# Performance work log

Measured on AMD Instinct MI355X. Metric: run time of the kernel, lower is better.

## Reference

```python
import jax, jax.numpy as jnp
import numpy as np

V = 50000
E = 640000
DIM = 128
NUM_EDGE_TYPES = 32


def setup_inputs() -> dict:
    key = jax.random.key(0)
    ks = jax.random.split(key, 8)
    return {
        "node_values": jax.random.normal(ks[0], (V, DIM), dtype=jnp.float32),
        "edge_src": jax.random.randint(ks[1], (E,), 0, V, dtype=jnp.int32),
        "edge_dest": jax.random.randint(ks[2], (E,), 0, V, dtype=jnp.int32),
        "edge_cls": jax.random.randint(ks[3], (E,), 0, NUM_EDGE_TYPES, dtype=jnp.int32),
        "W_src": jax.random.normal(ks[4], (DIM, DIM), dtype=jnp.float32) / np.sqrt(DIM),
        "b_src": jnp.zeros((DIM,), dtype=jnp.float32),
        "W_dest": jax.random.normal(ks[5], (DIM, DIM), dtype=jnp.float32) / np.sqrt(DIM),
        "b_dest": jnp.zeros((DIM,), dtype=jnp.float32),
        "edge_emb": jax.random.normal(ks[6], (NUM_EDGE_TYPES, DIM), dtype=jnp.float32),
    }


def reference(node_values, edge_src, edge_dest, edge_cls, W_src, b_src, W_dest, b_dest, edge_emb):
    # Dense projections over all nodes, then gather per edge (matches tf.gather(dense(...), idx))
    src_proj = node_values @ W_src + b_src    # [V, dim]
    dest_proj = node_values @ W_dest + b_dest  # [V, dim]
    # Per-edge fused message: gather src, gather dest, edge-class embedding lookup, add, relu
    msgs = jax.nn.relu(src_proj[edge_src] + dest_proj[edge_dest] + edge_emb[edge_cls])  # [E, dim]
    # Scatter-reduce messages onto destination nodes
    out = jax.ops.segment_sum(msgs, edge_dest, num_segments=V)  # [V, dim]
    return out
```

## Files before the change

### kernel.cpp

```cpp
#include <hip/hip_runtime.h>


#define V 50000
#define E 640000
#define DIM 128
#define NRES 4
#define DRANGE 12500
#define NBIN_R 100
#define BINW 125
#define NBINS 400
#define BINCAP 2048
#define NE_MAX 896
#define QCAP 384
#define NCHUNK 256
#define EC4 625
#define NPROJ 782
#define NFUSED 1806

typedef __bf16 bf16x8 __attribute__((ext_vector_type(8)));
typedef float  f32x4  __attribute__((ext_vector_type(4)));
typedef float  f32x2  __attribute__((ext_vector_type(2)));

__device__ __forceinline__ float bf2f(unsigned int u16) {
    union { unsigned int i; float f; } c; c.i = u16 << 16; return c.f;
}
__device__ __forceinline__ unsigned int f2bf(float f) {
    union { float f; unsigned int i; } c; c.f = f;
    unsigned int u = c.i;
    return (u + 0x7FFFu + ((u >> 16) & 1u)) >> 16;
}

__global__ __launch_bounds__(256) void mp_setup(
    const float* __restrict__ Ws, const float* __restrict__ Wd,
    const float* __restrict__ emb,
    unsigned short* __restrict__ Wpk, unsigned short* __restrict__ embB,
    int* __restrict__ binCnt)
{
    int tid = blockIdx.x * 256 + threadIdx.x;
    int mat  = tid >> 11;
    int rem  = tid & 2047;
    int ct   = rem >> 8;
    int kt   = (rem >> 6) & 3;
    int lane = rem & 63;
    const float* W = mat ? Wd : Ws;
    int n  = ct * 16 + (lane & 15);
    int k0 = kt * 32 + (lane >> 4) * 8;
    unsigned short* dst = Wpk + (size_t)tid * 8;
    #pragma unroll
    for (int j = 0; j < 8; ++j) dst[j] = (unsigned short)f2bf(W[(k0 + j) * DIM + n]);
    embB[tid] = (unsigned short)f2bf(emb[tid]);
    if (tid < NBINS) binCnt[tid] = 0;
}

__global__ __launch_bounds__(256) void mp_fused(
    const int* __restrict__ ed, const int* __restrict__ es, const int* __restrict__ ec,
    int* __restrict__ binCnt, int* __restrict__ binbuf,
    const float* __restrict__ x, const unsigned short* __restrict__ Wpk,
    const float* __restrict__ bs, const float* __restrict__ bd,
    unsigned char* __restrict__ ps8, unsigned short* __restrict__ pdB)
{
    __shared__ float stage[4][16 * 132];

    const int b = blockIdx.x;
    const int t = threadIdx.x;
    const int r7 = b % 7;
    const bool isBin = (b < 1792) && (r7 < 4);

    if (isBin) {
        int* hist  = (int*)&stage[0][0];
        int* lofs  = hist + NBIN_R;
        int* lcur  = lofs + NBIN_R + 1;
        int* gbase = lcur + NBIN_R;
        int* csr   = gbase + NBIN_R;
        unsigned short* sbin = (unsigned short*)(csr + NE_MAX);

        const int a = (b / 7) * 4 + r7;
        const int r = a & (NRES - 1);
        const int c = a >> 2;
        const int dlo = r * DRANGE;

        if (t < NBIN_R) hist[t] = 0;

        int4 DV[3], SV[3], CV[3];
        {
            const int4* ed4 = (const int4*)ed + (size_t)c * EC4;
            const int4* es4 = (const int4*)es + (size_t)c * EC4;
            const int4* ec4 = (const int4*)ec + (size_t)c * EC4;
            #pragma unroll
            for (int k = 0; k < 3; ++k) {
                int i = t + k * 256;
                if (i < EC4) { DV[k] = ed4[i]; SV[k] = es4[i]; CV[k] = ec4[i]; }
                else { DV[k] = make_int4(-1, -1, -1, -1);
                       SV[k] = make_int4(0, 0, 0, 0); CV[k] = make_int4(0, 0, 0, 0); }
            }
        }
        __syncthreads();

        #pragma unroll
        for (int k = 0; k < 3; ++k) {
            #define H1(D) { int rel = (D) - dlo; \
                if ((unsigned)rel < DRANGE) atomicAdd(&hist[(unsigned)rel / BINW], 1); }
            H1(DV[k].x); H1(DV[k].y); H1(DV[k].z); H1(DV[k].w);
            #undef H1
        }
        __syncthreads();

        if (t < NBIN_R) gbase[t] = atomicAdd(&binCnt[r * NBIN_R + t], hist[t]);
        if (t < 64) {
            int carry = 0;
            #pragma unroll
            for (int s = 0; s < 2; ++s) {
                int idx = s * 64 + t;
                int v = (idx < NBIN_R) ? hist[idx] : 0;
                #pragma unroll
                for (int dlt = 1; dlt < 64; dlt <<= 1) {
                    int u = __shfl_up(v, dlt, 64);
                    if (t >= dlt) v += u;
                }
                int tot = __shfl(v, 63, 64);
                v += carry;
                if (idx < NBIN_R) { lofs[idx + 1] = v; lcur[idx] = v - hist[idx]; }
                carry += tot;
            }
            if (t == 0) lofs[0] = 0;
        }
        __syncthreads();

        #pragma unroll
        for (int k = 0; k < 3; ++k) {
            #define SC1(D, S, C) { int rel = (D) - dlo; \
                if ((unsigned)rel < DRANGE) { \
                    int bn = (unsigned)rel / BINW; \
                    int rl = rel - bn * BINW; \
                    int pos = atomicAdd(&lcur[bn], 1); \
                    if (pos < NE_MAX) { \
                        csr[pos] = ((S) & 0xFFFF) | ((C) << 16) | (rl << 21); \
                        sbin[pos] = (unsigned short)bn; } } }
            SC1(DV[k].x, SV[k].x, CV[k].x); SC1(DV[k].y, SV[k].y, CV[k].y);
            SC1(DV[k].z, SV[k].z, CV[k].z); SC1(DV[k].w, SV[k].w, CV[k].w);
            #undef SC1
        }
        __syncthreads();

        int ne = lofs[NBIN_R]; if (ne > NE_MAX) ne = NE_MAX;

        for (int i = t; i < ne; i += 256) {
            int bb = sbin[i];
            int slot = gbase[bb] + (i - lofs[bb]);
            if (slot < BINCAP)
                binbuf[(size_t)(r * NBIN_R + bb) * BINCAP + slot] = csr[i];
        }
        return;
    }

    const int p = (b < 1792) ? ((b / 7) * 3 + (r7 - 4)) : (768 + (b - 1792));
    if (p >= NPROJ) return;
    const int wave = __builtin_amdgcn_readfirstlane(threadIdx.x) >> 6;
    const int lane = threadIdx.x & 63;
    const int m = lane & 15, q = lane >> 4;
    const int row0 = p * 64 + wave * 16;

    int arow = row0 + m; if (arow >= V) arow = V - 1;
    const float* xr = x + (size_t)arow * DIM + q * 8;

    bf16x8 A[4];
    #pragma unroll
    for (int kt = 0; kt < 4; ++kt) {
        float4 u = *(const float4*)(xr + kt * 32);
        float4 v = *(const float4*)(xr + kt * 32 + 4);
        bf16x8 a;
        a[0] = (__bf16)u.x; a[1] = (__bf16)u.y; a[2] = (__bf16)u.z; a[3] = (__bf16)u.w;
        a[4] = (__bf16)v.x; a[5] = (__bf16)v.y; a[6] = (__bf16)v.z; a[7] = (__bf16)v.w;
        A[kt] = a;
    }

    const bf16x8* Bp = (const bf16x8*)Wpk;

    f32x4 accS[8], accD[8];
    #pragma unroll
    for (int ct = 0; ct < 8; ++ct) {
        f32x4 aS = {0.f, 0.f, 0.f, 0.f}, aD = {0.f, 0.f, 0.f, 0.f};
        #pragma unroll
        for (int kt = 0; kt < 4; ++kt) {
            bf16x8 bS = Bp[((0 * 8 + ct) * 4 + kt) * 64 + lane];
            bf16x8 bD = Bp[((1 * 8 + ct) * 4 + kt) * 64 + lane];
            aS = __builtin_amdgcn_mfma_f32_16x16x32_bf16(A[kt], bS, aS, 0, 0, 0);
            aD = __builtin_amdgcn_mfma_f32_16x16x32_bf16(A[kt], bD, aD, 0, 0, 0);
        }
        accS[ct] = aS; accD[ct] = aD;
    }

    float* st = stage[wave];
    const int rr = lane & 15, cg = lane >> 4;
    const int orow = row0 + rr;
    const float* rowp = st + rr * 132 + cg * 32;

    #pragma unroll
    for (int ct = 0; ct < 8; ++ct) {
        const float bv = bs[ct * 16 + m];
        #pragma unroll
        for (int rg = 0; rg < 4; ++rg)
            st[(q * 4 + rg) * 132 + ct * 16 + m] = accS[ct][rg] + bv;
    }
    __syncthreads();
    {
        int w[8];
        #pragma unroll
        for (int j = 0; j < 8; ++j) {
            float4 f = *(const float4*)(rowp + 4 * j);
            int v = __builtin_amdgcn_cvt_pk_fp8_f32(f.x, f.y, 0, false);
            v = __builtin_amdgcn_cvt_pk_fp8_f32(f.z, f.w, v, true);
            w[j] = v;
        }
        if (orow < V) {
            int4* dst = (int4*)(ps8 + (size_t)orow * 128 + cg * 32);
            dst[0] = make_int4(w[0], w[1], w[2], w[3]);
            dst[1] = make_int4(w[4], w[5], w[6], w[7]);
        }
    }
    __syncthreads();

    #pragma unroll
    for (int ct = 0; ct < 8; ++ct) {
        const float bv = bd[ct * 16 + m];
        #pragma unroll
        for (int rg = 0; rg < 4; ++rg)
            st[(q * 4 + rg) * 132 + ct * 16 + m] = accD[ct][rg] + bv;
    }
    __syncthreads();
    {
        int w[16];
        #pragma unroll
        for (int j = 0; j < 8; ++j) {
            float4 f = *(const float4*)(rowp + 4 * j);
            w[2 * j]     = f2bf(f.x) | (f2bf(f.y) << 16);
            w[2 * j + 1] = f2bf(f.z) | (f2bf(f.w) << 16);
        }
        if (orow < V) {
            int4* dst = (int4*)(pdB + (size_t)orow * 128 + cg * 32);
            #pragma unroll
            for (int jj = 0; jj < 4; ++jj)
                dst[jj] = make_int4(w[4 * jj], w[4 * jj + 1], w[4 * jj + 2], w[4 * jj + 3]);
        }
    }
}

__global__ __launch_bounds__(256) void mp_binBC(
    const unsigned char* __restrict__ ps8, const unsigned short* __restrict__ pdB,
    const unsigned short* __restrict__ embB,
    const int* __restrict__ binCnt, const int* __restrict__ binbuf,
    float* __restrict__ out)
{
    __shared__ int csr[QCAP];
    __shared__ int cnt[16];
    __shared__ int off[17];
    __shared__ int cur[16];
    __shared__ unsigned short sEmb[32 * DIM];

    const int bin = blockIdx.x >> 3;
    const int qu = blockIdx.x & 7;
    const int rel0 = qu * 16;
    const int relW = (qu == 7) ? 13 : 16;
    const int d0 = bin * BINW + rel0;
    const int t = threadIdx.x;
    const int wave = t >> 6, lane = t & 63;

    int nb = binCnt[bin]; if (nb > BINCAP) nb = BINCAP;
    const int* buf = binbuf + (size_t)bin * BINCAP;

    if (t < 16) cnt[t] = 0;

    {
        const int4* s4 = (const int4*)embB;
        int4* d4 = (int4*)sEmb;
        d4[t] = s4[t];
        d4[t + 256] = s4[t + 256];
    }

    int EB[8];
    #pragma unroll
    for (int k = 0; k < 8; ++k) {
        int i = t + k * 256;
        EB[k] = (i < nb) ? buf[i] : -1;
    }

    float dp0v[4], dp1v[4];
    #pragma unroll
    for (int k = 0; k < 4; ++k) {
        int rl = wave + k * 4;
        int d = d0 + ((rl < relW) ? rl : 0);
        unsigned int pdu = *(const unsigned int*)(pdB + (size_t)d * DIM + 2 * lane);
        dp0v[k] = bf2f(pdu & 0xFFFF); dp1v[k] = bf2f(pdu >> 16);
    }
    __syncthreads();

    #pragma unroll
    for (int k = 0; k < 8; ++k) {
        int rl = (int)((unsigned)EB[k] >> 21) - rel0;
        if ((unsigned)rl < (unsigned)relW) atomicAdd(&cnt[rl], 1);
    }
    __syncthreads();

    if (t < 16) {
        int v = (t < relW) ? cnt[t] : 0;
        #pragma unroll
        for (int dlt = 1; dlt < 16; dlt <<= 1) {
            int u = __shfl_up(v, dlt, 64);
            if (t >= dlt) v += u;
        }
        off[t + 1] = v;
        cur[t] = v - cnt[t];
        if (t == 0) off[0] = 0;
    }
    __syncthreads();

    #pragma unroll
    for (int k = 0; k < 8; ++k) {
        int rl = (int)((unsigned)EB[k] >> 21) - rel0;
        if ((unsigned)rl < (unsigned)relW) {
            int pos = atomicAdd(&cur[rl], 1);
            if (pos < QCAP) csr[pos] = EB[k];
        }
    }
    __syncthreads();

    #define PROC(P) { \
        int s_ = *(const unsigned short*)(ps8 + ((size_t)((P) & 0xFFFF) << 7) + 2 * lane); \
        unsigned int e_ = *(const unsigned int*)(sEmb + ((((P) >> 16) & 0x1F) << 7) + 2 * lane); \
        f32x2 f_ = __builtin_amdgcn_cvt_pk_f32_fp8(s_, false); \
        a0 += fmaxf(f_.x + dp0 + bf2f(e_ & 0xFFFF), 0.f); \
        a1 += fmaxf(f_.y + dp1 + bf2f(e_ >> 16),    0.f); }

    #pragma unroll
    for (int k = 0; k < 4; ++k) {
        const int rl = wave + k * 4;
        if (rl >= relW) break;
        const int d = d0 + rl;
        int i0 = off[rl], i1 = off[rl + 1];
        if (i1 > QCAP) i1 = QCAP;
        if (i0 > i1) i0 = i1;
        const float dp0 = dp0v[k], dp1 = dp1v[k];
        float a0 = 0.f, a1 = 0.f;
        int i = i0;
        for (; i + 8 <= i1; i += 8) {
            int p0 = csr[i],     p1 = csr[i + 1], p2 = csr[i + 2], p3 = csr[i + 3];
            int p4 = csr[i + 4], p5 = csr[i + 5], p6 = csr[i + 6], p7 = csr[i + 7];
            PROC(p0); PROC(p1); PROC(p2); PROC(p3);
            PROC(p4); PROC(p5); PROC(p6); PROC(p7);
        }
        for (; i + 4 <= i1; i += 4) {
            int p0 = csr[i], p1 = csr[i + 1], p2 = csr[i + 2], p3 = csr[i + 3];
            PROC(p0); PROC(p1); PROC(p2); PROC(p3);
        }
        for (; i < i1; ++i) { int p0 = csr[i]; PROC(p0); }
        *(float2*)(out + (size_t)d * DIM + 2 * lane) = make_float2(a0, a1);
    }
    #undef PROC
}

extern "C" void kernel_launch(void* const* d_in, const int* in_sizes, int n_in,
                              void* d_out, int out_size, void* d_ws, size_t ws_size,
                              hipStream_t stream) {
    const float* x   = (const float*)d_in[0];
    const int*   es  = (const int*)d_in[1];
    const int*   ed  = (const int*)d_in[2];
    const int*   ec  = (const int*)d_in[3];
    const float* Ws  = (const float*)d_in[4];
    const float* bs  = (const float*)d_in[5];
    const float* Wd  = (const float*)d_in[6];
    const float* bd  = (const float*)d_in[7];
    const float* emb = (const float*)d_in[8];
    float* out = (float*)d_out;

    char* ws = (char*)d_ws;
    size_t off = 0;
    unsigned char*  ps8  = (unsigned char*)(ws + off);  off += (size_t)V * 128;
    unsigned short* pdB  = (unsigned short*)(ws + off); off += (size_t)V * DIM * 2;
    int* binbuf = (int*)(ws + off);                     off += (size_t)NBINS * BINCAP * 4;
    int* binCnt = (int*)(ws + off);                     off += (size_t)NBINS * 4;
    unsigned short* Wpk  = (unsigned short*)(ws + off); off += 2 * 128 * 128 * 2;
    unsigned short* embB = (unsigned short*)(ws + off); off += 32 * 128 * 2;

    mp_setup<<<16, 256, 0, stream>>>(Ws, Wd, emb, Wpk, embB, binCnt);
    mp_fused<<<NFUSED, 256, 0, stream>>>(ed, es, ec, binCnt, binbuf,
                                         x, Wpk, bs, bd, ps8, pdB);
    mp_binBC<<<NBINS * 8, 256, 0, stream>>>(ps8, pdB, embB, binCnt, binbuf, out);
}
```

Measured before the change: 155.0 us.

## Bin all destinations per edge chunk in one pass and XCD-map bin blocks

```diff
diff --git a/kernel.cpp b/kernel.cpp
--- a/kernel.cpp
+++ b/kernel.cpp
@@ -4,18 +4,17 @@
 #define V 50000
 #define E 640000
 #define DIM 128
-#define NRES 4
-#define DRANGE 12500
-#define NBIN_R 100
+#define NXCD 8
+#define NBIN_R 50
 #define BINW 125
 #define NBINS 400
 #define BINCAP 2048
-#define NE_MAX 896
 #define QCAP 384
 #define NCHUNK 256
+#define CSRN 2500
 #define EC4 625
 #define NPROJ 782
-#define NFUSED 1806
+#define NFUSED 1038
 
 typedef __bf16 bf16x8 __attribute__((ext_vector_type(8)));
 typedef float  f32x4  __attribute__((ext_vector_type(4)));
@@ -63,23 +62,20 @@
 
     const int b = blockIdx.x;
     const int t = threadIdx.x;
-    const int r7 = b % 7;
-    const bool isBin = (b < 1792) && (r7 < 4);
+    const bool isBin = ((b & 3) == 3) && (b < 1024);
 
     if (isBin) {
-        int* hist  = (int*)&stage[0][0];
-        int* lofs  = hist + NBIN_R;
-        int* lcur  = lofs + NBIN_R + 1;
-        int* gbase = lcur + NBIN_R;
-        int* csr   = gbase + NBIN_R;
-        unsigned short* sbin = (unsigned short*)(csr + NE_MAX);
-
-        const int a = (b / 7) * 4 + r7;
-        const int r = a & (NRES - 1);
-        const int c = a >> 2;
-        const int dlo = r * DRANGE;
-
-        if (t < NBIN_R) hist[t] = 0;
+        int* base  = (int*)&stage[0][0];
+        int* hist  = base;
+        int* lofs  = base + 400;
+        int* lcur  = base + 801;
+        int* gbase = base + 1201;
+        int* csr   = base + 1601;
+        unsigned short* sbin = (unsigned short*)(base + 4101);
+
+        const int c = b >> 2;
+
+        for (int i = t; i < NBINS; i += 256) hist[i] = 0;
 
         int4 DV[3], SV[3], CV[3];
         {
@@ -98,20 +94,20 @@
 
         #pragma unroll
         for (int k = 0; k < 3; ++k) {
-            #define H1(D) { int rel = (D) - dlo; \
-                if ((unsigned)rel < DRANGE) atomicAdd(&hist[(unsigned)rel / BINW], 1); }
+            #define H1(D) if ((D) >= 0) atomicAdd(&hist[(unsigned)(D) / BINW], 1);
             H1(DV[k].x); H1(DV[k].y); H1(DV[k].z); H1(DV[k].w);
             #undef H1
         }
         __syncthreads();
 
-        if (t < NBIN_R) gbase[t] = atomicAdd(&binCnt[r * NBIN_R + t], hist[t]);
+        for (int i = t; i < NBINS; i += 256)
+            gbase[i] = atomicAdd(&binCnt[i], hist[i]);
         if (t < 64) {
             int carry = 0;
             #pragma unroll
-            for (int s = 0; s < 2; ++s) {
+            for (int s = 0; s < 7; ++s) {
                 int idx = s * 64 + t;
-                int v = (idx < NBIN_R) ? hist[idx] : 0;
+                int v = (idx < NBINS) ? hist[idx] : 0;
                 #pragma unroll
                 for (int dlt = 1; dlt < 64; dlt <<= 1) {
                     int u = __shfl_up(v, dlt, 64);
@@ -119,7 +115,7 @@
                 }
                 int tot = __shfl(v, 63, 64);
                 v += carry;
-                if (idx < NBIN_R) { lofs[idx + 1] = v; lcur[idx] = v - hist[idx]; }
+                if (idx < NBINS) { lofs[idx + 1] = v; lcur[idx] = v - hist[idx]; }
                 carry += tot;
             }
             if (t == 0) lofs[0] = 0;
@@ -128,32 +124,28 @@
 
         #pragma unroll
         for (int k = 0; k < 3; ++k) {
-            #define SC1(D, S, C) { int rel = (D) - dlo; \
-                if ((unsigned)rel < DRANGE) { \
-                    int bn = (unsigned)rel / BINW; \
-                    int rl = rel - bn * BINW; \
-                    int pos = atomicAdd(&lcur[bn], 1); \
-                    if (pos < NE_MAX) { \
-                        csr[pos] = ((S) & 0xFFFF) | ((C) << 16) | (rl << 21); \
-                        sbin[pos] = (unsigned short)bn; } } }
+            #define SC1(D, S, C) if ((D) >= 0) { \
+                int bn = (unsigned)(D) / BINW; \
+                int rl = (D) - bn * BINW; \
+                int pos = atomicAdd(&lcur[bn], 1); \
+                csr[pos] = ((S) & 0xFFFF) | ((C) << 16) | (rl << 21); \
+                sbin[pos] = (unsigned short)bn; }
             SC1(DV[k].x, SV[k].x, CV[k].x); SC1(DV[k].y, SV[k].y, CV[k].y);
             SC1(DV[k].z, SV[k].z, CV[k].z); SC1(DV[k].w, SV[k].w, CV[k].w);
             #undef SC1
         }
         __syncthreads();
 
-        int ne = lofs[NBIN_R]; if (ne > NE_MAX) ne = NE_MAX;
-
-        for (int i = t; i < ne; i += 256) {
+        for (int i = t; i < CSRN; i += 256) {
             int bb = sbin[i];
             int slot = gbase[bb] + (i - lofs[bb]);
             if (slot < BINCAP)
-                binbuf[(size_t)(r * NBIN_R + bb) * BINCAP + slot] = csr[i];
+                binbuf[(size_t)bb * BINCAP + slot] = csr[i];
         }
         return;
     }
 
-    const int p = (b < 1792) ? ((b / 7) * 3 + (r7 - 4)) : (768 + (b - 1792));
+    const int p = (b < 1024) ? (b - ((b + 1) >> 2)) : (b - 256);
     if (p >= NPROJ) return;
     const int wave = __builtin_amdgcn_readfirstlane(threadIdx.x) >> 6;
     const int lane = threadIdx.x & 63;
@@ -255,10 +247,12 @@
     __shared__ int cnt[16];
     __shared__ int off[17];
     __shared__ int cur[16];
-    __shared__ unsigned short sEmb[32 * DIM];
-
-    const int bin = blockIdx.x >> 3;
-    const int qu = blockIdx.x & 7;
+
+    const int r = blockIdx.x & (NXCD - 1);
+    const int rest = blockIdx.x >> 3;
+    const int bi = rest % NBIN_R;
+    const int qu = rest / NBIN_R;
+    const int bin = r * NBIN_R + bi;
     const int rel0 = qu * 16;
     const int relW = (qu == 7) ? 13 : 16;
     const int d0 = bin * BINW + rel0;
@@ -270,13 +264,6 @@
 
     if (t < 16) cnt[t] = 0;
 
-    {
-        const int4* s4 = (const int4*)embB;
-        int4* d4 = (int4*)sEmb;
-        d4[t] = s4[t];
-        d4[t + 256] = s4[t + 256];
-    }
-
     int EB[8];
     #pragma unroll
     for (int k = 0; k < 8; ++k) {
@@ -326,7 +313,7 @@
 
     #define PROC(P) { \
         int s_ = *(const unsigned short*)(ps8 + ((size_t)((P) & 0xFFFF) << 7) + 2 * lane); \
-        unsigned int e_ = *(const unsigned int*)(sEmb + ((((P) >> 16) & 0x1F) << 7) + 2 * lane); \
+        unsigned int e_ = *(const unsigned int*)(embB + ((((P) >> 16) & 0x1F) << 7) + 2 * lane); \
         f32x2 f_ = __builtin_amdgcn_cvt_pk_f32_fp8(s_, false); \
         a0 += fmaxf(f_.x + dp0 + bf2f(e_ & 0xFFFF), 0.f); \
         a1 += fmaxf(f_.y + dp1 + bf2f(e_ >> 16),    0.f); }
@@ -384,5 +371,5 @@
     mp_setup<<<16, 256, 0, stream>>>(Ws, Wd, emb, Wpk, embB, binCnt);
     mp_fused<<<NFUSED, 256, 0, stream>>>(ed, es, ec, binCnt, binbuf,
                                          x, Wpk, bs, bd, ps8, pdB);
-    mp_binBC<<<NBINS * 8, 256, 0, stream>>>(ps8, pdB, embB, binCnt, binbuf, out);
-}
+    mp_binBC<<<NBIN_R * NXCD * 8, 256, 0, stream>>>(ps8, pdB, embB, binCnt, binbuf, out);
+}
```

Result: faster. 147.5 us (-4.8%).
